# Optimization experiments

Hardware: AMD Instinct MI355X
Metric: run time of the kernel (lower is better)

Reference implementation:

```python
import jax, jax.numpy as jnp
import numpy as np

B = 8          # batch
RES = 64       # resolution (H = W)
DIM = 512      # channels
HEADS = 8
HD = DIM // HEADS   # 64
HSP, WSP = RES, 8   # idx=0: H_sp=resolution, W_sp=split_size
NH, NW = RES // HSP, RES // WSP   # windows per axis


def setup_inputs() -> dict:
    key = jax.random.key(0)
    k1, k2, k3 = jax.random.split(key, 3)
    qkv = jax.random.normal(k1, (3, B, RES * RES, DIM), dtype=jnp.float32)
    lepe_w = jax.random.normal(k2, (DIM, 1, 3, 3), dtype=jnp.float32) * 0.1
    lepe_b = jax.random.normal(k3, (DIM,), dtype=jnp.float32) * 0.1
    return {"qkv": qkv, "lepe_w": lepe_w, "lepe_b": lepe_b}


def _to_windows(t):
    # [B, L, C] row-major -> [B*NH*NW, HSP*WSP, C]; equivalent to the
    # block-diagonal flex_attention mask grouping (y//H_sp, x//W_sp).
    t = t.reshape(B, NH, HSP, NW, WSP, DIM)
    return t.transpose(0, 1, 3, 2, 4, 5).reshape(B * NH * NW, HSP * WSP, DIM)


def _from_windows(t):
    t = t.reshape(B, NH, NW, HSP, WSP, DIM).transpose(0, 1, 3, 2, 4, 5)
    return t.reshape(B, RES * RES, DIM)


def reference(qkv, lepe_w, lepe_b):
    q, k, v = qkv[0], qkv[1], qkv[2]            # each [B, L, C]
    qw, kw, vw = _to_windows(q), _to_windows(k), _to_windows(v)

    # LePE: depthwise 3x3 conv on v laid out per-window as [n, C, HSP, WSP]
    vimg = vw.transpose(0, 2, 1).reshape(-1, DIM, HSP, WSP)
    lepe = jax.lax.conv_general_dilated(
        vimg, lepe_w, window_strides=(1, 1), padding='SAME',
        dimension_numbers=('NCHW', 'OIHW', 'NCHW'), feature_group_count=DIM)
    lepe = lepe + lepe_b[None, :, None, None]
    lepe = lepe.reshape(-1, DIM, HSP * WSP).transpose(0, 2, 1)  # [n, T, C]

    def split_heads(t):
        return t.reshape(t.shape[0], t.shape[1], HEADS, HD)

    qh, kh, vh, lh = map(split_heads, (qw, kw, vw, lepe))
    scale = 1.0 / np.sqrt(HD).astype(np.float32)  # flex_attention default scale
    scores = jnp.einsum('wqhd,wkhd->whqk', qh, kh) * scale
    attn = jax.nn.softmax(scores, axis=-1)
    out = jnp.einsum('whqk,wkhd->wqhd', attn, vh) + lh   # [n, T, H, hd]
    out = out.reshape(out.shape[0], out.shape[1], DIM)
    return _from_windows(out)
```

## Files before the change

kernel.cpp:

```cpp
#include <hip/hip_runtime.h>
#include <hip/hip_bf16.h>

#define DIMV 512
#define HDV  64
#define KRING_B 32768
#define VT_BASE KRING_B
#define SMEM_B (VT_BASE + 65536)

typedef __bf16 bf16x8_t __attribute__((ext_vector_type(8)));
typedef float f32x4_t __attribute__((ext_vector_type(4)));

union Frag { bf16x8_t v; unsigned short u[8]; unsigned int w[4]; uint2 d[2]; uint4 q; };

static __device__ __forceinline__ unsigned short f2bf(float f) {
  return __builtin_bit_cast(unsigned short, (__bf16)f);
}
static __device__ __forceinline__ float bf2f(unsigned int h) {
  return __builtin_bit_cast(float, h << 16);
}
static __device__ __forceinline__ uint2 pack4(const float4 f) {
  uint2 r;
  r.x = (unsigned)f2bf(f.x) | ((unsigned)f2bf(f.y) << 16);
  r.y = (unsigned)f2bf(f.z) | ((unsigned)f2bf(f.w) << 16);
  return r;
}

#define BARRIER_NODRAIN() asm volatile("s_waitcnt lgkmcnt(0)\n\ts_barrier" ::: "memory")

__global__ __launch_bounds__(1024, 2)
void lepe_attn_kernel(const float* __restrict__ qkv,
                      const float* __restrict__ lw,
                      const float* __restrict__ lb,
                      float* __restrict__ out)
{
  __shared__ __align__(16) unsigned char smem[SMEM_B];

  const int head = blockIdx.x & 7;
  const int win  = blockIdx.x >> 3;
  const int bat  = win >> 3;
  const int nw   = win & 7;

  const int tid  = threadIdx.x;
  const int wave = tid >> 6, lane = tid & 63;
  const int l15  = lane & 15, g = lane >> 4;

  const float* qptr = qkv;
  const float* kptr = qkv + 16777216;
  const float* vptr = qkv + 33554432;
  const int rowbase = bat * 4096;

  auto grow = [&](int tok) -> int {
    return rowbase + ((tok >> 3) << 6) + (nw << 3) + (tok & 7);
  };

  const int s_t = tid >> 4;
  const int s_c = (tid & 15) * 4;
  const size_t GSTRIDE = 262144;
  const float* kg = kptr + (size_t)grow(s_t) * DIMV + head * HDV + s_c;
  const float* vg = vptr + (size_t)grow(s_t) * DIMV + head * HDV + s_c;

  const int lr   = s_t & 31;
  const int kwb0 = (s_t >> 5) * 4096 + (lr >> 4) * 2048 + (s_c >> 5) * 1024
                 + ((lr & 15) + 16 * ((s_c >> 3) & 3)) * 16 + (s_c & 7) * 2;

  float4 ck0, ck1, cv0, cv1;
  auto issueC = [&](int c) {
    ck0 = *(const float4*)(kg + (size_t)(2 * c) * GSTRIDE);
    ck1 = *(const float4*)(kg + (size_t)(2 * c + 1) * GSTRIDE);
    cv0 = *(const float4*)(vg + (size_t)(2 * c) * GSTRIDE);
    cv1 = *(const float4*)(vg + (size_t)(2 * c + 1) * GSTRIDE);
  };
  auto writeC = [&](int c) {
    unsigned char* slot = smem + (c & 1) * 16384;
    *(uint2*)(slot + kwb0)        = pack4(ck0);
    *(uint2*)(slot + 8192 + kwb0) = pack4(ck1);
    #pragma unroll
    for (int gi = 0; gi < 2; ++gi) {
      const float4 vv = gi ? cv1 : cv0;
      const int t2 = 2 * ((2 * c + gi) * 64 + s_t);
      float fv[4] = {vv.x, vv.y, vv.z, vv.w};
      #pragma unroll
      for (int i = 0; i < 4; ++i) {
        const int d = s_c + i;
        *(unsigned short*)(smem + VT_BASE + d * 1024 + (t2 ^ ((d & 7) << 4))) = f2bf(fv[i]);
      }
    }
  };

  issueC(0);

  const float QSC = 0.1803368801f;
  const int qbase = wave * 32;
  float4 qin[8];
  #pragma unroll
  for (int qi = 0; qi < 2; ++qi) {
    const float* qp = qptr + (size_t)grow(qbase + qi * 16 + l15) * DIMV + head * HDV;
    #pragma unroll
    for (int kc = 0; kc < 2; ++kc) {
      qin[qi * 4 + kc * 2 + 0] = *(const float4*)(qp + kc * 32 + 8 * g);
      qin[qi * 4 + kc * 2 + 1] = *(const float4*)(qp + kc * 32 + 8 * g + 4);
    }
  }

  writeC(0);

  Frag qf[2][2];
  #pragma unroll
  for (int qi = 0; qi < 2; ++qi)
    #pragma unroll
    for (int kc = 0; kc < 2; ++kc) {
      const float4 f0 = qin[qi * 4 + kc * 2 + 0];
      const float4 f1 = qin[qi * 4 + kc * 2 + 1];
      qf[qi][kc].u[0] = f2bf(f0.x * QSC); qf[qi][kc].u[1] = f2bf(f0.y * QSC);
      qf[qi][kc].u[2] = f2bf(f0.z * QSC); qf[qi][kc].u[3] = f2bf(f0.w * QSC);
      qf[qi][kc].u[4] = f2bf(f1.x * QSC); qf[qi][kc].u[5] = f2bf(f1.y * QSC);
      qf[qi][kc].u[6] = f2bf(f1.z * QSC); qf[qi][kc].u[7] = f2bf(f1.w * QSC);
    }

  __syncthreads();

  const f32x4_t zero4 = {0.f, 0.f, 0.f, 0.f};
  f32x4_t ot[4][2];
  #pragma unroll
  for (int di = 0; di < 4; ++di)
    #pragma unroll
    for (int qi = 0; qi < 2; ++qi) ot[di][qi] = zero4;
  float lsum[2] = {0.f, 0.f};

  const int vswz = (l15 & 7) << 4;

  #pragma unroll
  for (int c = 0; c < 4; ++c) {
    if (c < 3) issueC(c + 1);

    #pragma unroll
    for (int t4 = 0; t4 < 4; ++t4) {
      const int kt = c * 4 + t4;
      const unsigned char* kbase = smem + (c & 1) * 16384 + t4 * 4096 + lane * 16;

      Frag kf[2][2];
      #pragma unroll
      for (int ki = 0; ki < 2; ++ki)
        #pragma unroll
        for (int kc = 0; kc < 2; ++kc)
          kf[ki][kc].q = *(const uint4*)(kbase + ki * 2048 + kc * 1024);

      f32x4_t st[2][2];
      #pragma unroll
      for (int ki = 0; ki < 2; ++ki)
        #pragma unroll
        for (int qi = 0; qi < 2; ++qi) st[ki][qi] = zero4;

      __builtin_amdgcn_s_setprio(1);
      #pragma unroll
      for (int kc = 0; kc < 2; ++kc)
        #pragma unroll
        for (int ki = 0; ki < 2; ++ki)
          #pragma unroll
          for (int qi = 0; qi < 2; ++qi)
            st[ki][qi] = __builtin_amdgcn_mfma_f32_16x16x32_bf16(
                kf[ki][kc].v, qf[qi][kc].v, st[ki][qi], 0, 0, 0);
      __builtin_amdgcn_s_setprio(0);

      #pragma unroll
      for (int ki = 0; ki < 2; ++ki)
        #pragma unroll
        for (int qi = 0; qi < 2; ++qi) {
          f32x4_t s = st[ki][qi];
          #pragma unroll
          for (int r = 0; r < 4; ++r) {
            float pr = __builtin_amdgcn_exp2f(s[r]);
            s[r] = pr;
            lsum[qi] += pr;
          }
          st[ki][qi] = s;
        }

      Frag vf[4];
      #pragma unroll
      for (int di = 0; di < 4; ++di) {
        const unsigned char* vrow = smem + VT_BASE + (di * 16 + l15) * 1024;
        vf[di].d[0] = *(const uint2*)(vrow + ((kt * 64 + 8 * g) ^ vswz));
        vf[di].d[1] = *(const uint2*)(vrow + ((kt * 64 + 32 + 8 * g) ^ vswz));
      }

      __builtin_amdgcn_s_setprio(1);
      #pragma unroll
      for (int qi = 0; qi < 2; ++qi) {
        Frag pb;
        #pragma unroll
        for (int r = 0; r < 4; ++r) {
          pb.u[r]     = f2bf(st[0][qi][r]);
          pb.u[4 + r] = f2bf(st[1][qi][r]);
        }
        #pragma unroll
        for (int di = 0; di < 4; ++di)
          ot[di][qi] = __builtin_amdgcn_mfma_f32_16x16x32_bf16(
              vf[di].v, pb.v, ot[di][qi], 0, 0, 0);
      }
      __builtin_amdgcn_s_setprio(0);
    }

    if (c < 3) { writeC(c + 1); BARRIER_NODRAIN(); }
  }

  float rl[2];
  #pragma unroll
  for (int qi = 0; qi < 2; ++qi) {
    float s = lsum[qi];
    s += __shfl_xor(s, 16, 64);
    s += __shfl_xor(s, 32, 64);
    rl[qi] = 1.0f / s;
  }

  float lout[32];
  {
    float wgt[9];
    const float* wp = lw + (size_t)(head * HDV + lane) * 9;
    #pragma unroll
    for (int i = 0; i < 9; ++i) wgt[i] = wp[i];
    const float bias = lb[head * HDV + lane];
    const int yb = wave * 4;
    const unsigned char* vrow = smem + VT_BASE + lane * 1024;
    const int lsw = (lane & 7) << 4;

    float rm[8], rc[8], rp2[8];
    auto loadrow = [&](int y, float* dst) {
      if ((unsigned)y < 64u) {
        uint4 a = *(const uint4*)(vrow + ((y * 16) ^ lsw));
        dst[0] = bf2f(a.x & 0xffffu); dst[1] = bf2f(a.x >> 16);
        dst[2] = bf2f(a.y & 0xffffu); dst[3] = bf2f(a.y >> 16);
        dst[4] = bf2f(a.z & 0xffffu); dst[5] = bf2f(a.z >> 16);
        dst[6] = bf2f(a.w & 0xffffu); dst[7] = bf2f(a.w >> 16);
      } else {
        #pragma unroll
        for (int x = 0; x < 8; ++x) dst[x] = 0.f;
      }
    };
    loadrow(yb - 1, rm);
    loadrow(yb, rc);
    #pragma unroll
    for (int yy = 0; yy < 4; ++yy) {
      loadrow(yb + yy + 1, rp2);
      #pragma unroll
      for (int x = 0; x < 8; ++x) {
        float acc = bias;
        if (x > 0) acc += rm[x-1]*wgt[0] + rc[x-1]*wgt[3] + rp2[x-1]*wgt[6];
        acc += rm[x]*wgt[1] + rc[x]*wgt[4] + rp2[x]*wgt[7];
        if (x < 7) acc += rm[x+1]*wgt[2] + rc[x+1]*wgt[5] + rp2[x+1]*wgt[8];
        lout[yy * 8 + x] = acc;
      }
      #pragma unroll
      for (int x = 0; x < 8; ++x) { rm[x] = rc[x]; rc[x] = rp2[x]; }
    }
  }

  BARRIER_NODRAIN();

  #pragma unroll
  for (int t = 0; t < 32; ++t) {
    const int tok = qbase + t;
    *(unsigned short*)(smem + VT_BASE + tok * 128 + ((2 * lane) ^ ((tok & 7) << 4)))
        = f2bf(lout[t]);
  }
  BARRIER_NODRAIN();

  #pragma unroll
  for (int qi = 0; qi < 2; ++qi) {
    const float rlq = rl[qi];
    const int tok = qbase + qi * 16 + l15;
    const unsigned char* brow = smem + VT_BASE + tok * 128;
    const int bsw = (l15 & 7) << 4;
    float* op = out + (size_t)grow(tok) * DIMV + head * HDV;
    #pragma unroll
    for (int di = 0; di < 4; ++di) {
      uint2 lv = *(const uint2*)(brow + ((di * 32 + 8 * g) ^ bsw));
      float4 o;
      o.x = ot[di][qi][0] * rlq + bf2f(lv.x & 0xffffu);
      o.y = ot[di][qi][1] * rlq + bf2f(lv.x >> 16);
      o.z = ot[di][qi][2] * rlq + bf2f(lv.y & 0xffffu);
      o.w = ot[di][qi][3] * rlq + bf2f(lv.y >> 16);
      *(float4*)(op + di * 16 + 4 * g) = o;
    }
  }
}

extern "C" void kernel_launch(void* const* d_in, const int* in_sizes, int n_in,
                              void* d_out, int out_size, void* d_ws, size_t ws_size,
                              hipStream_t stream) {
  const float* qkv = (const float*)d_in[0];
  const float* lw  = (const float*)d_in[1];
  const float* lb  = (const float*)d_in[2];
  float* out = (float*)d_out;
  (void)in_sizes; (void)n_in; (void)out_size; (void)d_ws; (void)ws_size;

  dim3 grid(512);
  dim3 block(1024);
  hipLaunchKernelGGL(lepe_attn_kernel, grid, block, 0, stream, qkv, lw, lb, out);
}
```

Measured before the change: 85.48 us.

## Preload all V upfront, pad V layout, double-buffer LDS fragment loads

Loads the whole V tile from global memory at the start instead of streaming it per chunk, and stores V transposed with a padded row stride (524 bf16) in place of an XOR swizzle. The K and V fragment reads from LDS are double-buffered so the next tile's loads are issued before the current tile's MFMAs, and the LePE staging buffer moves to a per-wave padded region. It also raises the launch-bounds hint from 2 to 4, which pressures register allocation and may cause spills given the extra fragment registers.

```diff
diff --git a/kernel.cpp b/kernel.cpp
--- a/kernel.cpp
+++ b/kernel.cpp
@@ -3,9 +3,10 @@
 
 #define DIMV 512
 #define HDV  64
+#define VSTR 524
 #define KRING_B 32768
 #define VT_BASE KRING_B
-#define SMEM_B (VT_BASE + 65536)
+#define SMEM_B (VT_BASE + 64 * VSTR * 2)
 
 typedef __bf16 bf16x8_t __attribute__((ext_vector_type(8)));
 typedef float f32x4_t __attribute__((ext_vector_type(4)));
@@ -27,7 +28,7 @@
 
 #define BARRIER_NODRAIN() asm volatile("s_waitcnt lgkmcnt(0)\n\ts_barrier" ::: "memory")
 
-__global__ __launch_bounds__(1024, 2)
+__global__ __launch_bounds__(1024, 4)
 void lepe_attn_kernel(const float* __restrict__ qkv,
                       const float* __restrict__ lw,
                       const float* __restrict__ lb,
@@ -63,31 +64,21 @@
   const int kwb0 = (s_t >> 5) * 4096 + (lr >> 4) * 2048 + (s_c >> 5) * 1024
                  + ((lr & 15) + 16 * ((s_c >> 3) & 3)) * 16 + (s_c & 7) * 2;
 
-  float4 ck0, ck1, cv0, cv1;
-  auto issueC = [&](int c) {
+  float4 ck0, ck1;
+  auto issueK = [&](int c) {
     ck0 = *(const float4*)(kg + (size_t)(2 * c) * GSTRIDE);
     ck1 = *(const float4*)(kg + (size_t)(2 * c + 1) * GSTRIDE);
-    cv0 = *(const float4*)(vg + (size_t)(2 * c) * GSTRIDE);
-    cv1 = *(const float4*)(vg + (size_t)(2 * c + 1) * GSTRIDE);
   };
-  auto writeC = [&](int c) {
+  auto writeK = [&](int c) {
     unsigned char* slot = smem + (c & 1) * 16384;
     *(uint2*)(slot + kwb0)        = pack4(ck0);
     *(uint2*)(slot + 8192 + kwb0) = pack4(ck1);
-    #pragma unroll
-    for (int gi = 0; gi < 2; ++gi) {
-      const float4 vv = gi ? cv1 : cv0;
-      const int t2 = 2 * ((2 * c + gi) * 64 + s_t);
-      float fv[4] = {vv.x, vv.y, vv.z, vv.w};
-      #pragma unroll
-      for (int i = 0; i < 4; ++i) {
-        const int d = s_c + i;
-        *(unsigned short*)(smem + VT_BASE + d * 1024 + (t2 ^ ((d & 7) << 4))) = f2bf(fv[i]);
-      }
-    }
   };
 
-  issueC(0);
+  issueK(0);
+  float4 vin[8];
+  #pragma unroll
+  for (int j = 0; j < 8; ++j) vin[j] = *(const float4*)(vg + (size_t)j * GSTRIDE);
 
   const float QSC = 0.1803368801f;
   const int qbase = wave * 32;
@@ -102,7 +93,15 @@
     }
   }
 
-  writeC(0);
+  writeK(0);
+  #pragma unroll
+  for (int j = 0; j < 8; ++j) {
+    const int t = j * 64 + s_t;
+    float fv[4] = {vin[j].x, vin[j].y, vin[j].z, vin[j].w};
+    #pragma unroll
+    for (int i = 0; i < 4; ++i)
+      *(unsigned short*)(smem + VT_BASE + (s_c + i) * 1048 + 2 * t) = f2bf(fv[i]);
+  }
 
   Frag qf[2][2];
   #pragma unroll
@@ -127,81 +126,91 @@
     for (int qi = 0; qi < 2; ++qi) ot[di][qi] = zero4;
   float lsum[2] = {0.f, 0.f};
 
-  const int vswz = (l15 & 7) << 4;
+  Frag kf[2][2][2];
+  Frag vf[2][4];
+
+#define LOADF(B, CC, T4, KT) do {                                             \
+    const unsigned char* kb_ = smem + ((CC) & 1) * 16384 + (T4) * 4096        \
+                               + lane * 16;                                   \
+    kf[B][0][0].q = *(const uint4*)(kb_);                                     \
+    kf[B][0][1].q = *(const uint4*)(kb_ + 1024);                              \
+    kf[B][1][0].q = *(const uint4*)(kb_ + 2048);                              \
+    kf[B][1][1].q = *(const uint4*)(kb_ + 3072);                              \
+    _Pragma("unroll")                                                         \
+    for (int di_ = 0; di_ < 4; ++di_) {                                       \
+      const unsigned char* vr_ = smem + VT_BASE + (di_ * 16 + l15) * 1048     \
+                                 + (KT) * 64 + 8 * g;                         \
+      vf[B][di_].d[0] = *(const uint2*)(vr_);                                 \
+      vf[B][di_].d[1] = *(const uint2*)(vr_ + 32);                            \
+    }                                                                         \
+  } while (0)
+
+#define COMPUTE(B) do {                                                       \
+    f32x4_t st[2][2];                                                         \
+    _Pragma("unroll")                                                         \
+    for (int ki_ = 0; ki_ < 2; ++ki_)                                         \
+      _Pragma("unroll")                                                       \
+      for (int qi_ = 0; qi_ < 2; ++qi_) st[ki_][qi_] = zero4;                 \
+    __builtin_amdgcn_s_setprio(1);                                            \
+    _Pragma("unroll")                                                         \
+    for (int kc_ = 0; kc_ < 2; ++kc_)                                         \
+      _Pragma("unroll")                                                       \
+      for (int ki_ = 0; ki_ < 2; ++ki_)                                       \
+        _Pragma("unroll")                                                     \
+        for (int qi_ = 0; qi_ < 2; ++qi_)                                     \
+          st[ki_][qi_] = __builtin_amdgcn_mfma_f32_16x16x32_bf16(             \
+              kf[B][ki_][kc_].v, qf[qi_][kc_].v, st[ki_][qi_], 0, 0, 0);      \
+    __builtin_amdgcn_s_setprio(0);                                            \
+    _Pragma("unroll")                                                         \
+    for (int ki_ = 0; ki_ < 2; ++ki_)                                         \
+      _Pragma("unroll")                                                       \
+      for (int qi_ = 0; qi_ < 2; ++qi_) {                                     \
+        f32x4_t s_ = st[ki_][qi_];                                            \
+        _Pragma("unroll")                                                     \
+        for (int r_ = 0; r_ < 4; ++r_) {                                      \
+          float p_ = __builtin_amdgcn_exp2f(s_[r_]);                          \
+          s_[r_] = p_;                                                        \
+          lsum[qi_] += p_;                                                    \
+        }                                                                     \
+        st[ki_][qi_] = s_;                                                    \
+      }                                                                       \
+    __builtin_amdgcn_s_setprio(1);                                            \
+    _Pragma("unroll")                                                         \
+    for (int qi_ = 0; qi_ < 2; ++qi_) {                                       \
+      Frag pb_;                                                               \
+      _Pragma("unroll")                                                       \
+      for (int r_ = 0; r_ < 4; ++r_) {                                        \
+        pb_.u[r_]     = f2bf(st[0][qi_][r_]);                                 \
+        pb_.u[4 + r_] = f2bf(st[1][qi_][r_]);                                 \
+      }                                                                       \
+      _Pragma("unroll")                                                       \
+      for (int di_ = 0; di_ < 4; ++di_)                                       \
+        ot[di_][qi_] = __builtin_amdgcn_mfma_f32_16x16x32_bf16(               \
+            vf[B][di_].v, pb_.v, ot[di_][qi_], 0, 0, 0);                      \
+    }                                                                         \
+    __builtin_amdgcn_s_setprio(0);                                            \
+  } while (0)
+
+  LOADF(0, 0, 0, 0);
 
   #pragma unroll
   for (int c = 0; c < 4; ++c) {
-    if (c < 3) issueC(c + 1);
+    if (c < 3) issueK(c + 1);
 
     #pragma unroll
     for (int t4 = 0; t4 < 4; ++t4) {
       const int kt = c * 4 + t4;
-      const unsigned char* kbase = smem + (c & 1) * 16384 + t4 * 4096 + lane * 16;
-
-      Frag kf[2][2];
-      #pragma unroll
-      for (int ki = 0; ki < 2; ++ki)
-        #pragma unroll
-        for (int kc = 0; kc < 2; ++kc)
-          kf[ki][kc].q = *(const uint4*)(kbase + ki * 2048 + kc * 1024);
-
-      f32x4_t st[2][2];
-      #pragma unroll
-      for (int ki = 0; ki < 2; ++ki)
-        #pragma unroll
-        for (int qi = 0; qi < 2; ++qi) st[ki][qi] = zero4;
-
-      __builtin_amdgcn_s_setprio(1);
-      #pragma unroll
-      for (int kc = 0; kc < 2; ++kc)
-        #pragma unroll
-        for (int ki = 0; ki < 2; ++ki)
-          #pragma unroll
-          for (int qi = 0; qi < 2; ++qi)
-            st[ki][qi] = __builtin_amdgcn_mfma_f32_16x16x32_bf16(
-                kf[ki][kc].v, qf[qi][kc].v, st[ki][qi], 0, 0, 0);
-      __builtin_amdgcn_s_setprio(0);
-
-      #pragma unroll
-      for (int ki = 0; ki < 2; ++ki)
-        #pragma unroll
-        for (int qi = 0; qi < 2; ++qi) {
-          f32x4_t s = st[ki][qi];
-          #pragma unroll
-          for (int r = 0; r < 4; ++r) {
-            float pr = __builtin_amdgcn_exp2f(s[r]);
-            s[r] = pr;
-            lsum[qi] += pr;
-          }
-          st[ki][qi] = s;
-        }
-
-      Frag vf[4];
-      #pragma unroll
-      for (int di = 0; di < 4; ++di) {
-        const unsigned char* vrow = smem + VT_BASE + (di * 16 + l15) * 1024;
-        vf[di].d[0] = *(const uint2*)(vrow + ((kt * 64 + 8 * g) ^ vswz));
-        vf[di].d[1] = *(const uint2*)(vrow + ((kt * 64 + 32 + 8 * g) ^ vswz));
-      }
-
-      __builtin_amdgcn_s_setprio(1);
-      #pragma unroll
-      for (int qi = 0; qi < 2; ++qi) {
-        Frag pb;
-        #pragma unroll
-        for (int r = 0; r < 4; ++r) {
-          pb.u[r]     = f2bf(st[0][qi][r]);
-          pb.u[4 + r] = f2bf(st[1][qi][r]);
-        }
-        #pragma unroll
-        for (int di = 0; di < 4; ++di)
-          ot[di][qi] = __builtin_amdgcn_mfma_f32_16x16x32_bf16(
-              vf[di].v, pb.v, ot[di][qi], 0, 0, 0);
-      }
-      __builtin_amdgcn_s_setprio(0);
-    }
-
-    if (c < 3) { writeC(c + 1); BARRIER_NODRAIN(); }
+      if (t4 == 0) { LOADF(1, c, 1, kt + 1); COMPUTE(0); }
+      else if (t4 == 1) { LOADF(0, c, 2, kt + 1); COMPUTE(1); }
+      else if (t4 == 2) { LOADF(1, c, 3, kt + 1); COMPUTE(0); }
+      else { COMPUTE(1); }
+    }
+
+    if (c < 3) {
+      writeK(c + 1);
+      BARRIER_NODRAIN();
+      LOADF(0, c + 1, 0, (c + 1) * 4);
+    }
   }
 
   float rl[2];
@@ -221,13 +230,12 @@
     for (int i = 0; i < 9; ++i) wgt[i] = wp[i];
     const float bias = lb[head * HDV + lane];
     const int yb = wave * 4;
-    const unsigned char* vrow = smem + VT_BASE + lane * 1024;
-    const int lsw = (lane & 7) << 4;
+    const unsigned char* vrow = smem + VT_BASE + lane * 1048;
 
     float rm[8], rc[8], rp2[8];
     auto loadrow = [&](int y, float* dst) {
       if ((unsigned)y < 64u) {
-        uint4 a = *(const uint4*)(vrow + ((y * 16) ^ lsw));
+        uint4 a = *(const uint4*)(vrow + y * 16);
         dst[0] = bf2f(a.x & 0xffffu); dst[1] = bf2f(a.x >> 16);
         dst[2] = bf2f(a.y & 0xffffu); dst[3] = bf2f(a.y >> 16);
         dst[4] = bf2f(a.z & 0xffffu); dst[5] = bf2f(a.z >> 16);
@@ -257,24 +265,20 @@
 
   BARRIER_NODRAIN();
 
-  #pragma unroll
-  for (int t = 0; t < 32; ++t) {
-    const int tok = qbase + t;
-    *(unsigned short*)(smem + VT_BASE + tok * 128 + ((2 * lane) ^ ((tok & 7) << 4)))
-        = f2bf(lout[t]);
-  }
+  unsigned char* bp = smem + wave * 4352;
+  #pragma unroll
+  for (int t = 0; t < 32; ++t)
+    *(unsigned short*)(bp + t * 136 + 2 * lane) = f2bf(lout[t]);
   BARRIER_NODRAIN();
 
   #pragma unroll
   for (int qi = 0; qi < 2; ++qi) {
     const float rlq = rl[qi];
-    const int tok = qbase + qi * 16 + l15;
-    const unsigned char* brow = smem + VT_BASE + tok * 128;
-    const int bsw = (l15 & 7) << 4;
-    float* op = out + (size_t)grow(tok) * DIMV + head * HDV;
+    const int tl = qi * 16 + l15;
+    float* op = out + (size_t)grow(qbase + tl) * DIMV + head * HDV;
     #pragma unroll
     for (int di = 0; di < 4; ++di) {
-      uint2 lv = *(const uint2*)(brow + ((di * 32 + 8 * g) ^ bsw));
+      uint2 lv = *(const uint2*)(bp + tl * 136 + di * 32 + 8 * g);
       float4 o;
       o.x = ot[di][qi][0] * rlq + bf2f(lv.x & 0xffffu);
       o.y = ot[di][qi][1] * rlq + bf2f(lv.x >> 16);
@@ -283,6 +287,8 @@
       *(float4*)(op + di * 16 + 4 * g) = o;
     }
   }
+#undef LOADF
+#undef COMPUTE
 }
 
 extern "C" void kernel_launch(void* const* d_in, const int* in_sizes, int n_in,
```

Result: slower. 89.31 us (+4.5%).
